# Optimization experiments

Measured on AMD Instinct MI355X. Metric: run time of the kernel, lower is better.

The kernel has to match this reference:

```python
import jax, jax.numpy as jnp
import numpy as np

H = 256  # hidden_dim


def _bidir_lstm_layer(x, W_ih, W_hh, bias):
    """x: [S, B, in]; W_ih: [2, in, 4H]; W_hh: [2, H, 4H]; bias: [2, 4H].
    Returns [S, B, 2H] (forward || backward outputs per timestep).
    PyTorch gate order: i, f, g, o."""
    B = x.shape[1]
    init = (jnp.zeros((B, H), x.dtype), jnp.zeros((B, H), x.dtype))
    # precompute input projections for the whole sequence, both directions
    xp = jnp.einsum('sbi,dij->dsbj', x, W_ih) + bias[:, None, None, :]  # [2,S,B,4H]

    def make_step(W_hh_d):
        def step(carry, xt):
            h, c = carry
            g = xt + h @ W_hh_d  # [B, 4H]
            i = jax.nn.sigmoid(g[:, :H])
            f = jax.nn.sigmoid(g[:, H:2 * H])
            gg = jnp.tanh(g[:, 2 * H:3 * H])
            o = jax.nn.sigmoid(g[:, 3 * H:])
            c = f * c + i * gg
            h = o * jnp.tanh(c)
            return (h, c), h
        return step

    _, h_f = jax.lax.scan(make_step(W_hh[0]), init, xp[0])
    _, h_b = jax.lax.scan(make_step(W_hh[1]), init, xp[1], reverse=True)
    return jnp.concatenate([h_f, h_b], axis=-1)  # [S, B, 2H]


def setup_inputs() -> dict:
    key = jax.random.key(0)
    ks = jax.random.split(key, 11)
    s = 0.05  # small init scale to keep gates in their dynamic range
    inp = {
        'x': jax.random.normal(ks[0], (8192, 1024), jnp.float32),
        'w_ih0': jax.random.normal(ks[1], (2, 1024, 4 * H), jnp.float32) * s,
        'w_hh0': jax.random.normal(ks[2], (2, H, 4 * H), jnp.float32) * s,
        'b0': jax.random.normal(ks[3], (2, 4 * H), jnp.float32) * s,
        'w_ih': jax.random.normal(ks[4], (4, 2, 2 * H, 4 * H), jnp.float32) * s,
        'w_hh': jax.random.normal(ks[5], (4, 2, H, 4 * H), jnp.float32) * s,
        'b': jax.random.normal(ks[6], (4, 2, 4 * H), jnp.float32) * s,
        'w1': jax.random.normal(ks[7], (2 * H, 32), jnp.float32) * s,
        'b1': jax.random.normal(ks[8], (32,), jnp.float32) * s,
        'w2': jax.random.normal(ks[9], (32, 2), jnp.float32) * s,
        'b2': jax.random.normal(ks[10], (2,), jnp.float32) * s,
    }
    return inp


def reference(x, w_ih0, w_hh0, b0, w_ih, w_hh, b, w1, b1, w2, b2):
    # x: [S, 1024] -> [S, B=1, 1024] (module does unsqueeze(0).transpose(0,1))
    h = x[:, None, :]
    h = _bidir_lstm_layer(h, w_ih0, w_hh0, b0)
    for l in range(4):  # layers 1..4 (fixed count)
        h = _bidir_lstm_layer(h, w_ih[l], w_hh[l], b[l])
    # cat(forward output at last step, backward output at first step)
    feat = jnp.concatenate([h[-1, :, :H], h[0, :, H:]], axis=1)  # [1, 2H]
    out = (feat @ w1 + b1) @ w2 + b2  # [1, 2]
    return out
```

## Files before the change

### kernel.cpp

```cpp
#include <hip/hip_runtime.h>

constexpr int SQ = 8192;
constexpr int HD = 256;
constexpr int NG = 1024;

typedef __fp16 h2 __attribute__((ext_vector_type(2)));
typedef unsigned int uint;
typedef unsigned short ushort;

__device__ __forceinline__ float sigm_f(float x) {
  float e = __builtin_amdgcn_exp2f(-1.4426950408889634f * x);
  return __builtin_amdgcn_rcpf(1.0f + e);
}
__device__ __forceinline__ float tanh_f(float x) {
  float e = __builtin_amdgcn_exp2f(2.885390081777927f * x);
  return 1.0f - 2.0f * __builtin_amdgcn_rcpf(1.0f + e);
}
__device__ __forceinline__ h2 bch2(uint v) { return __builtin_bit_cast(h2, v); }
__device__ __forceinline__ uint pk(float a, float b) {
  return __builtin_bit_cast(uint, __builtin_amdgcn_cvt_pkrtz(a, b));
}
__device__ __forceinline__ float dpp_xor1(float x) {
  int v = __builtin_amdgcn_mov_dpp(__builtin_bit_cast(int, x), 0xB1, 0xF, 0xF, true);
  return __builtin_bit_cast(float, v);
}

__global__ __launch_bounds__(256) void gemm_xp(const float* __restrict__ A, int K,
                                               const float* __restrict__ W,
                                               const float* __restrict__ bias,
                                               float* __restrict__ out) {
  __shared__ float Al[16][64];
  __shared__ float Bl[16][64];
  const int tid = threadIdx.x;
  const int bm = blockIdx.x * 64;
  const int d  = blockIdx.y >> 4;
  const int bn = (blockIdx.y & 15) * 64;
  const float* Wd = W + (size_t)d * K * NG;
  const float* bd = bias + (size_t)d * NG;
  float* outd = out + (size_t)d * SQ * NG;

  const int m4 = (tid >> 4) << 2;
  const int n4 = (tid & 15) << 2;
  const int am = tid >> 2, ak = (tid & 3) << 2;
  const int bk = tid >> 4, bnn = (tid & 15) << 2;

  float acc[4][4] = {};
  for (int kt = 0; kt < K; kt += 16) {
    float4 av = *(const float4*)(A + (size_t)(bm + am) * K + kt + ak);
    float4 bv = *(const float4*)(Wd + (size_t)(kt + bk) * NG + bn + bnn);
    __syncthreads();
    Al[ak + 0][am] = av.x;
    Al[ak + 1][am] = av.y;
    Al[ak + 2][am] = av.z;
    Al[ak + 3][am] = av.w;
    *(float4*)&Bl[bk][bnn] = bv;
    __syncthreads();
#pragma unroll
    for (int k = 0; k < 16; ++k) {
      float4 a = *(const float4*)&Al[k][m4];
      float4 b = *(const float4*)&Bl[k][n4];
      float ar[4] = {a.x, a.y, a.z, a.w};
      float br[4] = {b.x, b.y, b.z, b.w};
#pragma unroll
      for (int i = 0; i < 4; ++i)
#pragma unroll
        for (int jj = 0; jj < 4; ++jj)
          acc[i][jj] = fmaf(ar[i], br[jj], acc[i][jj]);
    }
  }
#pragma unroll
  for (int i = 0; i < 4; ++i) {
    float4 o;
    o.x = acc[i][0] + bd[bn + n4 + 0];
    o.y = acc[i][1] + bd[bn + n4 + 1];
    o.z = acc[i][2] + bd[bn + n4 + 2];
    o.w = acc[i][3] + bd[bn + n4 + 3];
    *(float4*)(outd + (size_t)(bm + m4 + i) * NG + bn + n4) = o;
  }
}

__global__ __launch_bounds__(512, 1) void lstm_rec11(const float* __restrict__ Whh,
                                                     const float* __restrict__ xp,
                                                     float* __restrict__ obuf) {
  __shared__ uint4 wl[16 * 512];
  __shared__ uint  hl[2][128];
  const int d = blockIdx.x;
  const int j = threadIdx.x;
  const int u = j >> 1;
  const int s = j & 1;
  const float* W   = Whh + (size_t)d * HD * NG;
  const float* xpd = xp + (size_t)d * SQ * NG;

  for (int idx = j; idx < 16 * 512; idx += 512) {
    const int rem = idx & 511;
    const int uu  = rem >> 1;
    const int ss  = rem & 1;
    const int qq  = (idx >> 9) & 3;
    const int g   = idx >> 11;
    const int r0  = ss * 128 + 96 + 8 * qq;
    const int c   = g * 256 + uu;
    uint4 v;
    v.x = pk(W[(size_t)(r0 + 0) * NG + c], W[(size_t)(r0 + 1) * NG + c]);
    v.y = pk(W[(size_t)(r0 + 2) * NG + c], W[(size_t)(r0 + 3) * NG + c]);
    v.z = pk(W[(size_t)(r0 + 4) * NG + c], W[(size_t)(r0 + 5) * NG + c]);
    v.w = pk(W[(size_t)(r0 + 6) * NG + c], W[(size_t)(r0 + 7) * NG + c]);
    wl[idx] = v;
  }

  h2 wr[4][48];
#pragma unroll
  for (int g = 0; g < 4; ++g) {
    const float* Wc = W + (size_t)(s * 128) * NG + g * 256 + u;
#pragma unroll
    for (int k = 0; k < 48; ++k)
      wr[g][k] = __builtin_amdgcn_cvt_pkrtz(Wc[(size_t)(2 * k) * NG],
                                            Wc[(size_t)(2 * k + 1) * NG]);
  }

  if (j < 256) { ((uint*)hl)[j] = 0u; }
  __syncthreads();

  const int fwd = (d == 0) ? 1 : 0;
  int t = fwd ? 0 : SQ - 1;
  const int dt = fwd ? 1 : -1;
  float cc = 0.0f;
  int p = 0;

  float xc[4], xn[4] = {};
#pragma unroll
  for (int g = 0; g < 4; ++g) xc[g] = xpd[(size_t)t * NG + g * 256 + u];

  for (int step = 0; step < SQ; ++step) {
    if (step + 1 < SQ) {
#pragma unroll
      for (int g = 0; g < 4; ++g) xn[g] = xpd[(size_t)(t + dt) * NG + g * 256 + u];
    }

    const uint4* hb = (const uint4*)&hl[p][s * 64];
    float acc[4] = {0.0f, 0.0f, 0.0f, 0.0f};
#pragma unroll
    for (int q = 0; q < 12; ++q) {
      uint4 hq = hb[q];
      h2 hx = bch2(hq.x), hy = bch2(hq.y), hz = bch2(hq.z), hw = bch2(hq.w);
#pragma unroll
      for (int g = 0; g < 4; ++g) {
        acc[g] = __builtin_amdgcn_fdot2(wr[g][4 * q + 0], hx, acc[g], false);
        acc[g] = __builtin_amdgcn_fdot2(wr[g][4 * q + 1], hy, acc[g], false);
        acc[g] = __builtin_amdgcn_fdot2(wr[g][4 * q + 2], hz, acc[g], false);
        acc[g] = __builtin_amdgcn_fdot2(wr[g][4 * q + 3], hw, acc[g], false);
      }
    }
#pragma unroll
    for (int qq = 0; qq < 4; ++qq) {
      uint4 hq = hb[12 + qq];
      h2 hx = bch2(hq.x), hy = bch2(hq.y), hz = bch2(hq.z), hw = bch2(hq.w);
#pragma unroll
      for (int g = 0; g < 4; ++g) {
        uint4 wq = wl[(g * 4 + qq) * 512 + j];
        acc[g] = __builtin_amdgcn_fdot2(bch2(wq.x), hx, acc[g], false);
        acc[g] = __builtin_amdgcn_fdot2(bch2(wq.y), hy, acc[g], false);
        acc[g] = __builtin_amdgcn_fdot2(bch2(wq.z), hz, acc[g], false);
        acc[g] = __builtin_amdgcn_fdot2(bch2(wq.w), hw, acc[g], false);
      }
    }

#pragma unroll
    for (int g = 0; g < 4; ++g) acc[g] += dpp_xor1(acc[g]);

    float iv = sigm_f(acc[0] + xc[0]);
    float fv = sigm_f(acc[1] + xc[1]);
    float gv = tanh_f(acc[2] + xc[2]);
    float ov = sigm_f(acc[3] + xc[3]);
    cc = fv * cc + iv * gv;
    float hv = ov * tanh_f(cc);

    if (s == 0) {
      obuf[(size_t)t * 512 + (d << 8) + u] = hv;
      ((ushort*)hl[p ^ 1])[u] = (ushort)(pk(hv, hv) & 0xFFFFu);
    }

    asm volatile("s_waitcnt lgkmcnt(0)" ::: "memory");
    __builtin_amdgcn_s_barrier();
    __builtin_amdgcn_sched_barrier(0);

    p ^= 1;
#pragma unroll
    for (int g = 0; g < 4; ++g) xc[g] = xn[g];
    t += dt;
  }
}

__global__ void cls_k(const float* __restrict__ buf, const float* __restrict__ w1,
                      const float* __restrict__ b1, const float* __restrict__ w2,
                      const float* __restrict__ b2, float* __restrict__ out) {
  __shared__ float feat[512];
  __shared__ float hid[32];
  const int t = threadIdx.x;
  feat[t] = (t < 256) ? buf[(size_t)(SQ - 1) * 512 + t] : buf[t];
  __syncthreads();
  if (t < 32) {
    float a = b1[t];
    for (int k = 0; k < 512; ++k) a = fmaf(feat[k], w1[k * 32 + t], a);
    hid[t] = a;
  }
  __syncthreads();
  if (t < 2) {
    float a = b2[t];
    for (int k = 0; k < 32; ++k) a = fmaf(hid[k], w2[k * 2 + t], a);
    out[t] = a;
  }
}

extern "C" void kernel_launch(void* const* d_in, const int* in_sizes, int n_in,
                              void* d_out, int out_size, void* d_ws, size_t ws_size,
                              hipStream_t stream) {
  const float* x     = (const float*)d_in[0];
  const float* w_ih0 = (const float*)d_in[1];
  const float* w_hh0 = (const float*)d_in[2];
  const float* b0    = (const float*)d_in[3];
  const float* w_ih  = (const float*)d_in[4];
  const float* w_hh  = (const float*)d_in[5];
  const float* b     = (const float*)d_in[6];
  const float* w1    = (const float*)d_in[7];
  const float* b1    = (const float*)d_in[8];
  const float* w2    = (const float*)d_in[9];
  const float* b2    = (const float*)d_in[10];

  float* xp   = (float*)d_ws;
  float* bufA = xp + (size_t)2 * SQ * NG;
  float* bufB = bufA + (size_t)SQ * 512;

  const dim3 ggrid(SQ / 64, 32);

  gemm_xp<<<ggrid, 256, 0, stream>>>(x, 1024, w_ih0, b0, xp);
  lstm_rec11<<<2, 512, 0, stream>>>(w_hh0, xp, bufA);

  float* cur = bufA;
  float* nxt = bufB;
  for (int lyr = 0; lyr < 4; ++lyr) {
    gemm_xp<<<ggrid, 256, 0, stream>>>(cur, 512, w_ih + (size_t)lyr * 2 * 512 * 1024,
                                       b + (size_t)lyr * 2 * 1024, xp);
    lstm_rec11<<<2, 512, 0, stream>>>(w_hh + (size_t)lyr * 2 * 256 * 1024, xp, nxt);
    float* tmp = cur; cur = nxt; nxt = tmp;
  }

  cls_k<<<1, 512, 0, stream>>>(cur, w1, b1, w2, b2, (float*)d_out);
}
```

Measured before the change: 62.86 ms.

## Split LSTM recurrence K-halves across wave pairs with readlane h broadcast

The recurrent kernel is remapped so each wave handles 64 hidden units for one K-half, rather than pairing adjacent lanes. The h vector now goes through one LDS load per lane and readlane broadcasts from SGPRs, replacing repeated 16-byte LDS reads. The two K-halves are combined through an LDS partial-sum buffer and an extra barrier, replacing the DPP reduction. h is written back as packed pairs via DPP. This is meant to cut per-step LDS traffic, but it adds a second workgroup barrier on every timestep.

```diff
diff --git a/kernel.cpp b/kernel.cpp
--- a/kernel.cpp
+++ b/kernel.cpp
@@ -79,32 +79,35 @@
   }
 }
 
-__global__ __launch_bounds__(512, 1) void lstm_rec11(const float* __restrict__ Whh,
+__global__ __launch_bounds__(512, 1) void lstm_rec16(const float* __restrict__ Whh,
                                                      const float* __restrict__ xp,
                                                      float* __restrict__ obuf) {
   __shared__ uint4 wl[16 * 512];
   __shared__ uint  hl[2][128];
+  __shared__ float part[4][2][64][4];
   const int d = blockIdx.x;
   const int j = threadIdx.x;
-  const int u = j >> 1;
-  const int s = j & 1;
+  const int w = j >> 6;
+  const int l = j & 63;
+  const int pair = w >> 1;
+  const int s = w & 1;
+  const int u = pair * 64 + l;
   const float* W   = Whh + (size_t)d * HD * NG;
   const float* xpd = xp + (size_t)d * SQ * NG;
 
-  for (int idx = j; idx < 16 * 512; idx += 512) {
-    const int rem = idx & 511;
-    const int uu  = rem >> 1;
-    const int ss  = rem & 1;
-    const int qq  = (idx >> 9) & 3;
-    const int g   = idx >> 11;
-    const int r0  = ss * 128 + 96 + 8 * qq;
-    const int c   = g * 256 + uu;
-    uint4 v;
-    v.x = pk(W[(size_t)(r0 + 0) * NG + c], W[(size_t)(r0 + 1) * NG + c]);
-    v.y = pk(W[(size_t)(r0 + 2) * NG + c], W[(size_t)(r0 + 3) * NG + c]);
-    v.z = pk(W[(size_t)(r0 + 4) * NG + c], W[(size_t)(r0 + 5) * NG + c]);
-    v.w = pk(W[(size_t)(r0 + 6) * NG + c], W[(size_t)(r0 + 7) * NG + c]);
-    wl[idx] = v;
+#pragma unroll
+  for (int g = 0; g < 4; ++g) {
+#pragma unroll
+    for (int qq = 0; qq < 4; ++qq) {
+      const int r0 = s * 128 + 96 + 8 * qq;
+      const int c  = g * 256 + u;
+      uint4 v;
+      v.x = pk(W[(size_t)(r0 + 0) * NG + c], W[(size_t)(r0 + 1) * NG + c]);
+      v.y = pk(W[(size_t)(r0 + 2) * NG + c], W[(size_t)(r0 + 3) * NG + c]);
+      v.z = pk(W[(size_t)(r0 + 4) * NG + c], W[(size_t)(r0 + 5) * NG + c]);
+      v.w = pk(W[(size_t)(r0 + 6) * NG + c], W[(size_t)(r0 + 7) * NG + c]);
+      wl[(g * 4 + qq) * 512 + j] = v;
+    }
   }
 
   h2 wr[4][48];
@@ -117,7 +120,7 @@
                                             Wc[(size_t)(2 * k + 1) * NG]);
   }
 
-  if (j < 256) { ((uint*)hl)[j] = 0u; }
+  if (j < 256) ((uint*)hl)[j] = 0u;
   __syncthreads();
 
   const int fwd = (d == 0) ? 1 : 0;
@@ -136,47 +139,73 @@
       for (int g = 0; g < 4; ++g) xn[g] = xpd[(size_t)(t + dt) * NG + g * 256 + u];
     }
 
-    const uint4* hb = (const uint4*)&hl[p][s * 64];
-    float acc[4] = {0.0f, 0.0f, 0.0f, 0.0f};
-#pragma unroll
-    for (int q = 0; q < 12; ++q) {
-      uint4 hq = hb[q];
-      h2 hx = bch2(hq.x), hy = bch2(hq.y), hz = bch2(hq.z), hw = bch2(hq.w);
-#pragma unroll
-      for (int g = 0; g < 4; ++g) {
-        acc[g] = __builtin_amdgcn_fdot2(wr[g][4 * q + 0], hx, acc[g], false);
-        acc[g] = __builtin_amdgcn_fdot2(wr[g][4 * q + 1], hy, acc[g], false);
-        acc[g] = __builtin_amdgcn_fdot2(wr[g][4 * q + 2], hz, acc[g], false);
-        acc[g] = __builtin_amdgcn_fdot2(wr[g][4 * q + 3], hw, acc[g], false);
+    uint4 vh = *(const uint4*)&hl[p][s * 64 + (l & 15) * 4];
+
+    float acc0 = 0.0f, acc1 = 0.0f, acc2 = 0.0f, acc3 = 0.0f;
+#pragma unroll
+    for (int k = 0; k < 48; ++k) {
+      const int comp = k & 3, lane = k >> 2;
+      uint hk;
+      if      (comp == 0) hk = (uint)__builtin_amdgcn_readlane(__builtin_bit_cast(int, vh.x), lane);
+      else if (comp == 1) hk = (uint)__builtin_amdgcn_readlane(__builtin_bit_cast(int, vh.y), lane);
+      else if (comp == 2) hk = (uint)__builtin_amdgcn_readlane(__builtin_bit_cast(int, vh.z), lane);
+      else                hk = (uint)__builtin_amdgcn_readlane(__builtin_bit_cast(int, vh.w), lane);
+      h2 hh = bch2(hk);
+      acc0 = __builtin_amdgcn_fdot2(wr[0][k], hh, acc0, false);
+      acc1 = __builtin_amdgcn_fdot2(wr[1][k], hh, acc1, false);
+      acc2 = __builtin_amdgcn_fdot2(wr[2][k], hh, acc2, false);
+      acc3 = __builtin_amdgcn_fdot2(wr[3][k], hh, acc3, false);
+    }
+#pragma unroll
+    for (int qq = 0; qq < 4; ++qq) {
+      uint4 wq0 = wl[(0 * 4 + qq) * 512 + j];
+      uint4 wq1 = wl[(1 * 4 + qq) * 512 + j];
+      uint4 wq2 = wl[(2 * 4 + qq) * 512 + j];
+      uint4 wq3 = wl[(3 * 4 + qq) * 512 + j];
+#pragma unroll
+      for (int kk = 0; kk < 4; ++kk) {
+        const int k = 48 + qq * 4 + kk;
+        const int comp = k & 3, lane = k >> 2;
+        uint hk;
+        if      (comp == 0) hk = (uint)__builtin_amdgcn_readlane(__builtin_bit_cast(int, vh.x), lane);
+        else if (comp == 1) hk = (uint)__builtin_amdgcn_readlane(__builtin_bit_cast(int, vh.y), lane);
+        else if (comp == 2) hk = (uint)__builtin_amdgcn_readlane(__builtin_bit_cast(int, vh.z), lane);
+        else                hk = (uint)__builtin_amdgcn_readlane(__builtin_bit_cast(int, vh.w), lane);
+        h2 hh = bch2(hk);
+        const uint w0c = (kk == 0) ? wq0.x : (kk == 1) ? wq0.y : (kk == 2) ? wq0.z : wq0.w;
+        const uint w1c = (kk == 0) ? wq1.x : (kk == 1) ? wq1.y : (kk == 2) ? wq1.z : wq1.w;
+        const uint w2c = (kk == 0) ? wq2.x : (kk == 1) ? wq2.y : (kk == 2) ? wq2.z : wq2.w;
+        const uint w3c = (kk == 0) ? wq3.x : (kk == 1) ? wq3.y : (kk == 2) ? wq3.z : wq3.w;
+        acc0 = __builtin_amdgcn_fdot2(bch2(w0c), hh, acc0, false);
+        acc1 = __builtin_amdgcn_fdot2(bch2(w1c), hh, acc1, false);
+        acc2 = __builtin_amdgcn_fdot2(bch2(w2c), hh, acc2, false);
+        acc3 = __builtin_amdgcn_fdot2(bch2(w3c), hh, acc3, false);
       }
     }
-#pragma unroll
-    for (int qq = 0; qq < 4; ++qq) {
-      uint4 hq = hb[12 + qq];
-      h2 hx = bch2(hq.x), hy = bch2(hq.y), hz = bch2(hq.z), hw = bch2(hq.w);
-#pragma unroll
-      for (int g = 0; g < 4; ++g) {
-        uint4 wq = wl[(g * 4 + qq) * 512 + j];
-        acc[g] = __builtin_amdgcn_fdot2(bch2(wq.x), hx, acc[g], false);
-        acc[g] = __builtin_amdgcn_fdot2(bch2(wq.y), hy, acc[g], false);
-        acc[g] = __builtin_amdgcn_fdot2(bch2(wq.z), hz, acc[g], false);
-        acc[g] = __builtin_amdgcn_fdot2(bch2(wq.w), hw, acc[g], false);
-      }
-    }
-
-#pragma unroll
-    for (int g = 0; g < 4; ++g) acc[g] += dpp_xor1(acc[g]);
-
-    float iv = sigm_f(acc[0] + xc[0]);
-    float fv = sigm_f(acc[1] + xc[1]);
-    float gv = tanh_f(acc[2] + xc[2]);
-    float ov = sigm_f(acc[3] + xc[3]);
+
+    *(float4*)&part[pair][s][l][0] = make_float4(acc0, acc1, acc2, acc3);
+    asm volatile("s_waitcnt lgkmcnt(0)" ::: "memory");
+    __builtin_amdgcn_s_barrier();
+    __builtin_amdgcn_sched_barrier(0);
+
+    float4 po = *(const float4*)&part[pair][s ^ 1][l][0];
+    float pre0 = acc0 + po.x + xc[0];
+    float pre1 = acc1 + po.y + xc[1];
+    float pre2 = acc2 + po.z + xc[2];
+    float pre3 = acc3 + po.w + xc[3];
+
+    float iv = sigm_f(pre0);
+    float fv = sigm_f(pre1);
+    float gv = tanh_f(pre2);
+    float ov = sigm_f(pre3);
     cc = fv * cc + iv * gv;
     float hv = ov * tanh_f(cc);
 
     if (s == 0) {
       obuf[(size_t)t * 512 + (d << 8) + u] = hv;
-      ((ushort*)hl[p ^ 1])[u] = (ushort)(pk(hv, hv) & 0xFFFFu);
+      float hn = dpp_xor1(hv);
+      if (!(l & 1))
+        hl[p ^ 1][(u >> 1)] = pk(hv, hn);
     }
 
     asm volatile("s_waitcnt lgkmcnt(0)" ::: "memory");
@@ -233,14 +262,14 @@
   const dim3 ggrid(SQ / 64, 32);
 
   gemm_xp<<<ggrid, 256, 0, stream>>>(x, 1024, w_ih0, b0, xp);
-  lstm_rec11<<<2, 512, 0, stream>>>(w_hh0, xp, bufA);
+  lstm_rec16<<<2, 512, 0, stream>>>(w_hh0, xp, bufA);
 
   float* cur = bufA;
   float* nxt = bufB;
   for (int lyr = 0; lyr < 4; ++lyr) {
     gemm_xp<<<ggrid, 256, 0, stream>>>(cur, 512, w_ih + (size_t)lyr * 2 * 512 * 1024,
                                        b + (size_t)lyr * 2 * 1024, xp);
-    lstm_rec11<<<2, 512, 0, stream>>>(w_hh + (size_t)lyr * 2 * 256 * 1024, xp, nxt);
+    lstm_rec16<<<2, 512, 0, stream>>>(w_hh + (size_t)lyr * 2 * 256 * 1024, xp, nxt);
     float* tmp = cur; cur = nxt; nxt = tmp;
   }
 
```

New measurement: 74.70 ms. 18.8% more time.

## Split each LSTM direction across paired same-XCC blocks with flag-synced partial sums

Applied to the files above, without the earlier changes.

Each LSTM direction's recurrent matvec is now split over two workgroups. Each holds half the hidden-weight rows in registers, so the LDS-resident weight portion is gone. The blocks swap partial gate sums every timestep through global memory, using per-wave release/acquire flags. Blocks read their XCC id and pair up within the same XCC to keep the exchange in shared L2. This halves per-step FMA work but adds a cross-CU spin-wait handshake on every step, which may cost more than the compute saved.

```diff
diff --git a/kernel.cpp b/kernel.cpp
--- a/kernel.cpp
+++ b/kernel.cpp
@@ -79,50 +79,98 @@
   }
 }
 
-__global__ __launch_bounds__(512, 1) void lstm_rec11(const float* __restrict__ Whh,
-                                                     const float* __restrict__ xp,
-                                                     float* __restrict__ obuf) {
-  __shared__ uint4 wl[16 * 512];
-  __shared__ uint  hl[2][128];
-  const int d = blockIdx.x;
+__global__ void init_sync(int* flags, int* xcc) {
+  const int i = threadIdx.x;
+  if (i < 32) flags[i] = 0;
+  if (i < 80) xcc[i] = 0;
+}
+
+__global__ __launch_bounds__(512, 1) void lstm_pair(const float* __restrict__ Whh,
+                                                    const float* __restrict__ xp,
+                                                    float* __restrict__ obuf,
+                                                    float* gx, int* flags,
+                                                    int* xcc, int ep) {
+  __shared__ int  role_sh[2];
+  __shared__ uint hl[2][128];
+  __shared__ uint pad_[21504];
+
   const int j = threadIdx.x;
+  const int w = j >> 6;
+  const int l = j & 63;
+
+  if (j == 0) {
+    pad_[0] = 0u;
+    int myx;
+    asm volatile("s_getreg_b32 %0, hwreg(HW_REG_XCC_ID)" : "=s"(myx));
+    myx &= 7;
+    __hip_atomic_store(&xcc[blockIdx.x], myx + 1, __ATOMIC_RELEASE, __HIP_MEMORY_SCOPE_AGENT);
+    int ids[16];
+    for (int i = 0; i < 16; ++i) {
+      int v;
+      do { v = __hip_atomic_load(&xcc[i], __ATOMIC_ACQUIRE, __HIP_MEMORY_SCOPE_AGENT); } while (v == 0);
+      ids[i] = v - 1;
+    }
+    int pa[2][2] = {{-1, -1}, {-1, -1}};
+    int np = 0;
+    bool used[16];
+    for (int i = 0; i < 16; ++i) used[i] = false;
+    for (int x = 0; x < 8 && np < 2; ++x) {
+      int first = -1;
+      for (int i = 0; i < 16 && np < 2; ++i) {
+        if (!used[i] && ids[i] == x) {
+          if (first < 0) first = i;
+          else { pa[np][0] = first; pa[np][1] = i; used[first] = used[i] = true; ++np; first = -1; }
+        }
+      }
+    }
+    if (np < 2) {
+      int first = -1;
+      for (int i = 0; i < 16 && np < 2; ++i) {
+        if (!used[i]) {
+          if (first < 0) first = i;
+          else { pa[np][0] = first; pa[np][1] = i; used[first] = used[i] = true; ++np; first = -1; }
+        }
+      }
+    }
+    int rd = -1, rk = 0;
+    for (int dd = 0; dd < 2; ++dd)
+      for (int kk = 0; kk < 2; ++kk)
+        if (pa[dd][kk] == (int)blockIdx.x) { rd = dd; rk = kk; }
+    role_sh[0] = rd; role_sh[1] = rk;
+  }
+  __syncthreads();
+  const int d = role_sh[0];
+  const int k = role_sh[1];
+  if (d < 0) return;
+
   const int u = j >> 1;
   const int s = j & 1;
   const float* W   = Whh + (size_t)d * HD * NG;
   const float* xpd = xp + (size_t)d * SQ * NG;
-
-  for (int idx = j; idx < 16 * 512; idx += 512) {
-    const int rem = idx & 511;
-    const int uu  = rem >> 1;
-    const int ss  = rem & 1;
-    const int qq  = (idx >> 9) & 3;
-    const int g   = idx >> 11;
-    const int r0  = ss * 128 + 96 + 8 * qq;
-    const int c   = g * 256 + uu;
-    uint4 v;
-    v.x = pk(W[(size_t)(r0 + 0) * NG + c], W[(size_t)(r0 + 1) * NG + c]);
-    v.y = pk(W[(size_t)(r0 + 2) * NG + c], W[(size_t)(r0 + 3) * NG + c]);
-    v.z = pk(W[(size_t)(r0 + 4) * NG + c], W[(size_t)(r0 + 5) * NG + c]);
-    v.w = pk(W[(size_t)(r0 + 6) * NG + c], W[(size_t)(r0 + 7) * NG + c]);
-    wl[idx] = v;
-  }
-
-  h2 wr[4][48];
+  const int fd_self  = d * 2 + k;
+  const int fd_other = d * 2 + (1 - k);
+  float* gx_self  = gx + (size_t)fd_self  * 2 * 1024;
+  float* gx_other = gx + (size_t)fd_other * 2 * 1024;
+  int* flg_self  = flags + fd_self * 8 + w;
+  int* flg_other = flags + fd_other * 8 + w;
+
+  h2 wr[4][32];
 #pragma unroll
   for (int g = 0; g < 4; ++g) {
-    const float* Wc = W + (size_t)(s * 128) * NG + g * 256 + u;
-#pragma unroll
-    for (int k = 0; k < 48; ++k)
-      wr[g][k] = __builtin_amdgcn_cvt_pkrtz(Wc[(size_t)(2 * k) * NG],
-                                            Wc[(size_t)(2 * k + 1) * NG]);
-  }
-
-  if (j < 256) { ((uint*)hl)[j] = 0u; }
+    const float* Wc = W + (size_t)(k * 128 + s * 64) * NG + g * 256 + u;
+#pragma unroll
+    for (int m = 0; m < 32; ++m)
+      wr[g][m] = __builtin_amdgcn_cvt_pkrtz(Wc[(size_t)(2 * m) * NG],
+                                            Wc[(size_t)(2 * m + 1) * NG]);
+  }
+
+  if (j < 256) ((uint*)hl)[j] = 0u;
   __syncthreads();
 
   const int fwd = (d == 0) ? 1 : 0;
   int t = fwd ? 0 : SQ - 1;
   const int dt = fwd ? 1 : -1;
+  const int hqbase = k * 16 + s * 8;
   float cc = 0.0f;
   int p = 0;
 
@@ -131,16 +179,11 @@
   for (int g = 0; g < 4; ++g) xc[g] = xpd[(size_t)t * NG + g * 256 + u];
 
   for (int step = 0; step < SQ; ++step) {
-    if (step + 1 < SQ) {
-#pragma unroll
-      for (int g = 0; g < 4; ++g) xn[g] = xpd[(size_t)(t + dt) * NG + g * 256 + u];
-    }
-
-    const uint4* hb = (const uint4*)&hl[p][s * 64];
+    const uint4* hb = (const uint4*)hl[p];
     float acc[4] = {0.0f, 0.0f, 0.0f, 0.0f};
 #pragma unroll
-    for (int q = 0; q < 12; ++q) {
-      uint4 hq = hb[q];
+    for (int q = 0; q < 8; ++q) {
+      uint4 hq = hb[hqbase + q];
       h2 hx = bch2(hq.x), hy = bch2(hq.y), hz = bch2(hq.z), hw = bch2(hq.w);
 #pragma unroll
       for (int g = 0; g < 4; ++g) {
@@ -150,32 +193,48 @@
         acc[g] = __builtin_amdgcn_fdot2(wr[g][4 * q + 3], hw, acc[g], false);
       }
     }
-#pragma unroll
-    for (int qq = 0; qq < 4; ++qq) {
-      uint4 hq = hb[12 + qq];
-      h2 hx = bch2(hq.x), hy = bch2(hq.y), hz = bch2(hq.z), hw = bch2(hq.w);
-#pragma unroll
-      for (int g = 0; g < 4; ++g) {
-        uint4 wq = wl[(g * 4 + qq) * 512 + j];
-        acc[g] = __builtin_amdgcn_fdot2(bch2(wq.x), hx, acc[g], false);
-        acc[g] = __builtin_amdgcn_fdot2(bch2(wq.y), hy, acc[g], false);
-        acc[g] = __builtin_amdgcn_fdot2(bch2(wq.z), hz, acc[g], false);
-        acc[g] = __builtin_amdgcn_fdot2(bch2(wq.w), hw, acc[g], false);
-      }
-    }
-
-#pragma unroll
-    for (int g = 0; g < 4; ++g) acc[g] += dpp_xor1(acc[g]);
-
-    float iv = sigm_f(acc[0] + xc[0]);
-    float fv = sigm_f(acc[1] + xc[1]);
-    float gv = tanh_f(acc[2] + xc[2]);
-    float ov = sigm_f(acc[3] + xc[3]);
+
+    float part[4];
+#pragma unroll
+    for (int g = 0; g < 4; ++g) part[g] = acc[g] + dpp_xor1(acc[g]);
+
+    float* gxs = gx_self + (size_t)(step & 1) * 1024;
+    if (!(j & 1)) {
+#pragma unroll
+      for (int g = 0; g < 4; ++g)
+        __hip_atomic_store(gxs + g * 256 + u, part[g], __ATOMIC_RELAXED,
+                           __HIP_MEMORY_SCOPE_AGENT);
+    }
+    const int target = ep + step + 1;
+    if (l == 0)
+      __hip_atomic_store(flg_self, target, __ATOMIC_RELEASE, __HIP_MEMORY_SCOPE_AGENT);
+
+    if (step + 1 < SQ) {
+#pragma unroll
+      for (int g = 0; g < 4; ++g) xn[g] = xpd[(size_t)(t + dt) * NG + g * 256 + u];
+    }
+
+    while (__hip_atomic_load(flg_other, __ATOMIC_ACQUIRE, __HIP_MEMORY_SCOPE_AGENT) < target) {}
+    const float* gxo = gx_other + (size_t)(step & 1) * 1024;
+    float pre[4];
+#pragma unroll
+    for (int g = 0; g < 4; ++g) {
+      float po = __hip_atomic_load(gxo + g * 256 + u, __ATOMIC_RELAXED,
+                                   __HIP_MEMORY_SCOPE_AGENT);
+      float a = k ? po : part[g];
+      float b = k ? part[g] : po;
+      pre[g] = a + b + xc[g];
+    }
+
+    float iv = sigm_f(pre[0]);
+    float fv = sigm_f(pre[1]);
+    float gv = tanh_f(pre[2]);
+    float ov = sigm_f(pre[3]);
     cc = fv * cc + iv * gv;
     float hv = ov * tanh_f(cc);
 
-    if (s == 0) {
-      obuf[(size_t)t * 512 + (d << 8) + u] = hv;
+    if (!(j & 1)) {
+      if (k == 0) obuf[(size_t)t * 512 + (d << 8) + u] = hv;
       ((ushort*)hl[p ^ 1])[u] = (ushort)(pk(hv, hv) & 0xFFFFu);
     }
 
@@ -229,18 +288,24 @@
   float* xp   = (float*)d_ws;
   float* bufA = xp + (size_t)2 * SQ * NG;
   float* bufB = bufA + (size_t)SQ * 512;
+  float* gx   = bufB + (size_t)SQ * 512;
+  int*   flags = (int*)(gx + 4 * 2 * 1024);
+  int*   xcc   = flags + 32;
 
   const dim3 ggrid(SQ / 64, 32);
 
+  init_sync<<<1, 128, 0, stream>>>(flags, xcc);
+
   gemm_xp<<<ggrid, 256, 0, stream>>>(x, 1024, w_ih0, b0, xp);
-  lstm_rec11<<<2, 512, 0, stream>>>(w_hh0, xp, bufA);
+  lstm_pair<<<16, 512, 0, stream>>>(w_hh0, xp, bufA, gx, flags, xcc + 0 * 16, 0 * SQ);
 
   float* cur = bufA;
   float* nxt = bufB;
   for (int lyr = 0; lyr < 4; ++lyr) {
     gemm_xp<<<ggrid, 256, 0, stream>>>(cur, 512, w_ih + (size_t)lyr * 2 * 512 * 1024,
                                        b + (size_t)lyr * 2 * 1024, xp);
-    lstm_rec11<<<2, 512, 0, stream>>>(w_hh + (size_t)lyr * 2 * 256 * 1024, xp, nxt);
+    lstm_pair<<<16, 512, 0, stream>>>(w_hh + (size_t)lyr * 2 * 256 * 1024, xp, nxt,
+                                      gx, flags, xcc + (lyr + 1) * 16, (lyr + 1) * SQ);
     float* tmp = cur; cur = nxt; nxt = tmp;
   }
 
```

New measurement: 218.8 ms. 3.48x slower.

## Split LSTM recurrence K across four lanes, two hidden units per lane group

Applied to the files above, without the earlier changes.

Restructures the recurrent matvec so that four lanes share each pair of hidden units, each lane covering a quarter of K and all 8 gate columns. The partials are reduced with two DPP xor shuffles, and the h buffer in LDS is padded to 36 dwords per quarter to avoid bank conflicts. Each lane now reads 8 uint4 of h instead of 16, which shortens the LDS broadcast traffic on the serial critical path. The cost is an extra reduction shuffle stage and duplicated gate math across the four lanes.

```diff
diff --git a/kernel.cpp b/kernel.cpp
--- a/kernel.cpp
+++ b/kernel.cpp
@@ -22,6 +22,10 @@
 }
 __device__ __forceinline__ float dpp_xor1(float x) {
   int v = __builtin_amdgcn_mov_dpp(__builtin_bit_cast(int, x), 0xB1, 0xF, 0xF, true);
+  return __builtin_bit_cast(float, v);
+}
+__device__ __forceinline__ float dpp_xor2(float x) {
+  int v = __builtin_amdgcn_mov_dpp(__builtin_bit_cast(int, x), 0x4E, 0xF, 0xF, true);
   return __builtin_bit_cast(float, v);
 }
 
@@ -79,104 +83,121 @@
   }
 }
 
-__global__ __launch_bounds__(512, 1) void lstm_rec11(const float* __restrict__ Whh,
+__global__ __launch_bounds__(512, 1) void lstm_rec19(const float* __restrict__ Whh,
                                                      const float* __restrict__ xp,
                                                      float* __restrict__ obuf) {
   __shared__ uint4 wl[16 * 512];
-  __shared__ uint  hl[2][128];
+  __shared__ uint  hl[2][144];
   const int d = blockIdx.x;
   const int j = threadIdx.x;
-  const int u = j >> 1;
-  const int s = j & 1;
+  const int q = j & 3;
+  const int m = j >> 2;
   const float* W   = Whh + (size_t)d * HD * NG;
   const float* xpd = xp + (size_t)d * SQ * NG;
 
-  for (int idx = j; idx < 16 * 512; idx += 512) {
-    const int rem = idx & 511;
-    const int uu  = rem >> 1;
-    const int ss  = rem & 1;
-    const int qq  = (idx >> 9) & 3;
-    const int g   = idx >> 11;
-    const int r0  = ss * 128 + 96 + 8 * qq;
-    const int c   = g * 256 + uu;
-    uint4 v;
-    v.x = pk(W[(size_t)(r0 + 0) * NG + c], W[(size_t)(r0 + 1) * NG + c]);
-    v.y = pk(W[(size_t)(r0 + 2) * NG + c], W[(size_t)(r0 + 3) * NG + c]);
-    v.z = pk(W[(size_t)(r0 + 4) * NG + c], W[(size_t)(r0 + 5) * NG + c]);
-    v.w = pk(W[(size_t)(r0 + 6) * NG + c], W[(size_t)(r0 + 7) * NG + c]);
-    wl[idx] = v;
-  }
-
-  h2 wr[4][48];
-#pragma unroll
-  for (int g = 0; g < 4; ++g) {
-    const float* Wc = W + (size_t)(s * 128) * NG + g * 256 + u;
-#pragma unroll
-    for (int k = 0; k < 48; ++k)
-      wr[g][k] = __builtin_amdgcn_cvt_pkrtz(Wc[(size_t)(2 * k) * NG],
-                                            Wc[(size_t)(2 * k + 1) * NG]);
-  }
-
-  if (j < 256) { ((uint*)hl)[j] = 0u; }
+#pragma unroll
+  for (int cs = 0; cs < 8; ++cs) {
+    const int c = (cs >> 1) * 256 + m + (cs & 1) * 128;
+#pragma unroll
+    for (int t = 0; t < 2; ++t) {
+      const int r0 = 64 * q + 48 + 8 * t;
+      uint4 v;
+      v.x = pk(W[(size_t)(r0 + 0) * NG + c], W[(size_t)(r0 + 1) * NG + c]);
+      v.y = pk(W[(size_t)(r0 + 2) * NG + c], W[(size_t)(r0 + 3) * NG + c]);
+      v.z = pk(W[(size_t)(r0 + 4) * NG + c], W[(size_t)(r0 + 5) * NG + c]);
+      v.w = pk(W[(size_t)(r0 + 6) * NG + c], W[(size_t)(r0 + 7) * NG + c]);
+      wl[(cs * 2 + t) * 512 + j] = v;
+    }
+  }
+
+  h2 wr[8][24];
+#pragma unroll
+  for (int cs = 0; cs < 8; ++cs) {
+    const int c = (cs >> 1) * 256 + m + (cs & 1) * 128;
+    const float* Wc = W + (size_t)(64 * q) * NG + c;
+#pragma unroll
+    for (int k = 0; k < 24; ++k)
+      wr[cs][k] = __builtin_amdgcn_cvt_pkrtz(Wc[(size_t)(2 * k) * NG],
+                                             Wc[(size_t)(2 * k + 1) * NG]);
+  }
+
+  if (j < 288) ((uint*)hl)[j] = 0u;
   __syncthreads();
 
   const int fwd = (d == 0) ? 1 : 0;
   int t = fwd ? 0 : SQ - 1;
   const int dt = fwd ? 1 : -1;
-  float cc = 0.0f;
+  float cc0 = 0.0f, cc1 = 0.0f;
   int p = 0;
 
-  float xc[4], xn[4] = {};
-#pragma unroll
-  for (int g = 0; g < 4; ++g) xc[g] = xpd[(size_t)t * NG + g * 256 + u];
+  float xc[8], xn[8] = {};
+#pragma unroll
+  for (int cs = 0; cs < 8; ++cs)
+    xc[cs] = xpd[(size_t)t * NG + (cs >> 1) * 256 + m + (cs & 1) * 128];
 
   for (int step = 0; step < SQ; ++step) {
     if (step + 1 < SQ) {
 #pragma unroll
-      for (int g = 0; g < 4; ++g) xn[g] = xpd[(size_t)(t + dt) * NG + g * 256 + u];
-    }
-
-    const uint4* hb = (const uint4*)&hl[p][s * 64];
-    float acc[4] = {0.0f, 0.0f, 0.0f, 0.0f};
-#pragma unroll
-    for (int q = 0; q < 12; ++q) {
-      uint4 hq = hb[q];
-      h2 hx = bch2(hq.x), hy = bch2(hq.y), hz = bch2(hq.z), hw = bch2(hq.w);
-#pragma unroll
-      for (int g = 0; g < 4; ++g) {
-        acc[g] = __builtin_amdgcn_fdot2(wr[g][4 * q + 0], hx, acc[g], false);
-        acc[g] = __builtin_amdgcn_fdot2(wr[g][4 * q + 1], hy, acc[g], false);
-        acc[g] = __builtin_amdgcn_fdot2(wr[g][4 * q + 2], hz, acc[g], false);
-        acc[g] = __builtin_amdgcn_fdot2(wr[g][4 * q + 3], hw, acc[g], false);
+      for (int cs = 0; cs < 8; ++cs)
+        xn[cs] = xpd[(size_t)(t + dt) * NG + (cs >> 1) * 256 + m + (cs & 1) * 128];
+    }
+
+    const uint4* hb = (const uint4*)&hl[p][q * 36];
+    float acc[8] = {};
+#pragma unroll
+    for (int i = 0; i < 6; ++i) {
+      uint4 hq = hb[i];
+      h2 h0 = bch2(hq.x), h1 = bch2(hq.y), h2v = bch2(hq.z), h3 = bch2(hq.w);
+#pragma unroll
+      for (int cs = 0; cs < 8; ++cs) {
+        acc[cs] = __builtin_amdgcn_fdot2(wr[cs][4 * i + 0], h0, acc[cs], false);
+        acc[cs] = __builtin_amdgcn_fdot2(wr[cs][4 * i + 1], h1, acc[cs], false);
+        acc[cs] = __builtin_amdgcn_fdot2(wr[cs][4 * i + 2], h2v, acc[cs], false);
+        acc[cs] = __builtin_amdgcn_fdot2(wr[cs][4 * i + 3], h3, acc[cs], false);
       }
     }
 #pragma unroll
-    for (int qq = 0; qq < 4; ++qq) {
-      uint4 hq = hb[12 + qq];
-      h2 hx = bch2(hq.x), hy = bch2(hq.y), hz = bch2(hq.z), hw = bch2(hq.w);
-#pragma unroll
-      for (int g = 0; g < 4; ++g) {
-        uint4 wq = wl[(g * 4 + qq) * 512 + j];
-        acc[g] = __builtin_amdgcn_fdot2(bch2(wq.x), hx, acc[g], false);
-        acc[g] = __builtin_amdgcn_fdot2(bch2(wq.y), hy, acc[g], false);
-        acc[g] = __builtin_amdgcn_fdot2(bch2(wq.z), hz, acc[g], false);
-        acc[g] = __builtin_amdgcn_fdot2(bch2(wq.w), hw, acc[g], false);
+    for (int tt = 0; tt < 2; ++tt) {
+      uint4 hq = hb[6 + tt];
+      h2 h0 = bch2(hq.x), h1 = bch2(hq.y), h2v = bch2(hq.z), h3 = bch2(hq.w);
+#pragma unroll
+      for (int cs = 0; cs < 8; ++cs) {
+        uint4 wq = wl[(cs * 2 + tt) * 512 + j];
+        acc[cs] = __builtin_amdgcn_fdot2(bch2(wq.x), h0, acc[cs], false);
+        acc[cs] = __builtin_amdgcn_fdot2(bch2(wq.y), h1, acc[cs], false);
+        acc[cs] = __builtin_amdgcn_fdot2(bch2(wq.z), h2v, acc[cs], false);
+        acc[cs] = __builtin_amdgcn_fdot2(bch2(wq.w), h3, acc[cs], false);
       }
     }
 
 #pragma unroll
-    for (int g = 0; g < 4; ++g) acc[g] += dpp_xor1(acc[g]);
-
-    float iv = sigm_f(acc[0] + xc[0]);
-    float fv = sigm_f(acc[1] + xc[1]);
-    float gv = tanh_f(acc[2] + xc[2]);
-    float ov = sigm_f(acc[3] + xc[3]);
-    cc = fv * cc + iv * gv;
-    float hv = ov * tanh_f(cc);
-
-    if (s == 0) {
-      obuf[(size_t)t * 512 + (d << 8) + u] = hv;
-      ((ushort*)hl[p ^ 1])[u] = (ushort)(pk(hv, hv) & 0xFFFFu);
+    for (int cs = 0; cs < 8; ++cs) {
+      acc[cs] += dpp_xor1(acc[cs]);
+      acc[cs] += dpp_xor2(acc[cs]);
+    }
+
+    float iv0 = sigm_f(acc[0] + xc[0]);
+    float iv1 = sigm_f(acc[1] + xc[1]);
+    float fv0 = sigm_f(acc[2] + xc[2]);
+    float fv1 = sigm_f(acc[3] + xc[3]);
+    float gv0 = tanh_f(acc[4] + xc[4]);
+    float gv1 = tanh_f(acc[5] + xc[5]);
+    float ov0 = sigm_f(acc[6] + xc[6]);
+    float ov1 = sigm_f(acc[7] + xc[7]);
+    cc0 = fv0 * cc0 + iv0 * gv0;
+    cc1 = fv1 * cc1 + iv1 * gv1;
+    float hv0 = ov0 * tanh_f(cc0);
+    float hv1 = ov1 * tanh_f(cc1);
+
+    if (q == 0) {
+      obuf[(size_t)t * 512 + (d << 8) + m] = hv0;
+      obuf[(size_t)t * 512 + (d << 8) + m + 128] = hv1;
+      ushort* hp = (ushort*)hl[p ^ 1];
+      const int u1 = m + 128;
+      const int dw0 = 36 * (m >> 6) + ((m >> 1) & 31);
+      const int dw1 = 36 * (u1 >> 6) + ((u1 >> 1) & 31);
+      hp[dw0 * 2 + (m & 1)]  = (ushort)(pk(hv0, hv0) & 0xFFFFu);
+      hp[dw1 * 2 + (u1 & 1)] = (ushort)(pk(hv1, hv1) & 0xFFFFu);
     }
 
     asm volatile("s_waitcnt lgkmcnt(0)" ::: "memory");
@@ -185,7 +206,7 @@
 
     p ^= 1;
 #pragma unroll
-    for (int g = 0; g < 4; ++g) xc[g] = xn[g];
+    for (int cs = 0; cs < 8; ++cs) xc[cs] = xn[cs];
     t += dt;
   }
 }
@@ -233,14 +254,14 @@
   const dim3 ggrid(SQ / 64, 32);
 
   gemm_xp<<<ggrid, 256, 0, stream>>>(x, 1024, w_ih0, b0, xp);
-  lstm_rec11<<<2, 512, 0, stream>>>(w_hh0, xp, bufA);
+  lstm_rec19<<<2, 512, 0, stream>>>(w_hh0, xp, bufA);
 
   float* cur = bufA;
   float* nxt = bufB;
   for (int lyr = 0; lyr < 4; ++lyr) {
     gemm_xp<<<ggrid, 256, 0, stream>>>(cur, 512, w_ih + (size_t)lyr * 2 * 512 * 1024,
                                        b + (size_t)lyr * 2 * 1024, xp);
-    lstm_rec11<<<2, 512, 0, stream>>>(w_hh + (size_t)lyr * 2 * 256 * 1024, xp, nxt);
+    lstm_rec19<<<2, 512, 0, stream>>>(w_hh + (size_t)lyr * 2 * 256 * 1024, xp, nxt);
     float* tmp = cur; cur = nxt; nxt = tmp;
   }
 
```

Result: slower. 71.44 ms (+13.6%).
